# Optimization experiments

Measured on AMD Instinct MI355X. Metric: run time of the kernel, lower is better.

The kernel has to match this reference:

```python
import jax, jax.numpy as jnp
import numpy as np

B, S, H = 8, 2048, 512
DK = 512


def setup_inputs() -> dict:
    key = jax.random.key(0)
    ks = jax.random.split(key, 10)
    inp = {
        "X": jax.random.normal(ks[0], (B, S, H), dtype=jnp.float32),
        "event_flag": jax.random.uniform(ks[1], (B, S, 1), dtype=jnp.float32),
        "lengths": jax.random.randint(ks[2], (B,), 1, S + 1),
        # Linear params (torch Linear: y = x @ W.T + b, W is [out,in])
        "Wq": jax.random.normal(ks[3], (H, H), dtype=jnp.float32) / np.sqrt(H),
        "bq": jnp.zeros((H,), dtype=jnp.float32),
        "Wk": jax.random.normal(ks[4], (H, H), dtype=jnp.float32) / np.sqrt(H),
        "bk": jnp.zeros((H,), dtype=jnp.float32),
        "Wv": jax.random.normal(ks[5], (H, H), dtype=jnp.float32) / np.sqrt(H),
        "bv": jnp.zeros((H,), dtype=jnp.float32),
        "event_weight": jnp.zeros((1,), dtype=jnp.float32),
        "shape_ratio": jnp.ones((1,), dtype=jnp.float32),
    }
    return inp


def reference(X, event_flag, lengths, Wq, bq, Wk, bk, Wv, bv, event_weight, shape_ratio):
    # QKV projections: [B,S,H]
    Q = jnp.einsum("bsh,oh->bso", X, Wq) + bq
    K = jnp.einsum("bsh,oh->bso", X, Wk) + bk
    V = jnp.einsum("bsh,oh->bso", X, Wv) + bv
    # scaled scores [B,S,S], learned shape_ratio scale
    scores = jnp.einsum("bqh,bkh->bqk", Q, K) / jnp.sqrt(jnp.float32(DK))
    scores = scores * shape_ratio
    # event_flag [B,S,1] broadcasts over last (key) dim: per-query additive bias
    scores = scores + event_weight * event_flag
    attn = jax.nn.softmax(scores, axis=-1)
    context = jnp.einsum("bqk,bkh->bqh", attn, V)
    return context, attn
```

## Files before the change

### kernel.cpp

```cpp
#include <hip/hip_runtime.h>
#include <stdint.h>


#define Bn 8
#define Sn 2048
#define Hn 512
#define BM 128
#define BN 128
#define BKk 64

typedef unsigned short u16;
typedef _Float16 h16;
typedef __attribute__((ext_vector_type(8))) _Float16 f16x8;
typedef __attribute__((ext_vector_type(4))) _Float16 f16x4;
typedef __attribute__((ext_vector_type(4))) float f32x4;

__device__ __forceinline__ f32x4 mfma16h(f16x8 a, f16x8 b, f32x4 c) {
  return __builtin_amdgcn_mfma_f32_16x16x32_f16(a, b, c, 0, 0, 0);
}
__device__ __forceinline__ void g2l16(const void* g, void* l) {
  __builtin_amdgcn_global_load_lds(
      (const __attribute__((address_space(1))) void*)g,
      (__attribute__((address_space(3))) void*)l,
      16, 0, 0);
}

__global__ __launch_bounds__(256) void k0_cvt(
    const float* __restrict__ X,
    const float* __restrict__ Wq, const float* __restrict__ Wk,
    const float* __restrict__ Wv,
    h16* __restrict__ Xf, h16* __restrict__ Wf) {
  const int l = blockIdx.x;
  const float* src;
  h16* dst;
  int i;
  if (l < 4096) {
    src = X;
    dst = Xf;
    i = (l * 256 + threadIdx.x) * 8;
  } else {
    const int w = l - 4096;
    const int mat = w >> 7;
    src = (mat == 0) ? Wq : ((mat == 1) ? Wk : Wv);
    dst = Wf + (size_t)mat * 512 * 512;
    i = ((w & 127) * 256 + threadIdx.x) * 8;
  }
  float4 v0 = *(const float4*)(src + i);
  float4 v1 = *(const float4*)(src + i + 4);
  f16x8 h;
  h[0] = (h16)v0.x; h[1] = (h16)v0.y; h[2] = (h16)v0.z; h[3] = (h16)v0.w;
  h[4] = (h16)v1.x; h[5] = (h16)v1.y; h[6] = (h16)v1.z; h[7] = (h16)v1.w;
  *(f16x8*)(dst + i) = h;
}

__global__ __launch_bounds__(256) void k1_proj(
    const h16* __restrict__ Xf, const h16* __restrict__ Wf,
    const float* __restrict__ bq, const float* __restrict__ bk,
    const float* __restrict__ bv,
    h16* __restrict__ Qf, h16* __restrict__ Kf, h16* __restrict__ Vt) {
  __shared__ h16 lA[BM * BKk], lB[BM * BKk];
  const int t = threadIdx.x;
  const int lane = t & 63;
  const int wid = t >> 6;
  const int wr = wid >> 1, wc = wid & 1;
  const int l = blockIdx.x;
  const int xcd = l & 7;
  const int slot = l >> 3;
  const int m_idx = xcd * 16 + slot / 12;
  const int tn = slot % 12;
  const int m0 = m_idx * BM;
  const int mat = tn >> 2;
  const int o0 = (tn & 3) * BN;
  const float* bsel = (mat == 0) ? bq : ((mat == 1) ? bk : bv);
  const size_t arow0 = (size_t)m0;
  const size_t brow0 = (size_t)mat * 512 + o0;

  f32x4 acc[4][4];
  const f32x4 fz = {0.f, 0.f, 0.f, 0.f};
#pragma unroll
  for (int m = 0; m < 4; ++m)
#pragma unroll
    for (int n = 0; n < 4; ++n) acc[m][n] = fz;

  const int srow = lane >> 3;
  const int scol = ((lane & 7) ^ srow) << 3;

  for (int k0 = 0; k0 < Hn; k0 += BKk) {
    __syncthreads();
#pragma unroll
    for (int j = 0; j < 4; ++j) {
      const int ci = wid * 4 + j;
      const int row = ci * 8 + srow;
      g2l16(Xf + (arow0 + row) * Hn + k0 + scol, &lA[ci * 512]);
      g2l16(Wf + (brow0 + row) * Hn + k0 + scol, &lB[ci * 512]);
    }
    __syncthreads();
#pragma unroll
    for (int ks = 0; ks < 2; ++ks) {
      f16x8 af[4], bf[4];
#pragma unroll
      for (int m = 0; m < 4; ++m) {
        const int row = wr * 64 + m * 16 + (lane & 15);
        const int col8 = ks * 4 + (lane >> 4);
        af[m] = *(const f16x8*)&lA[row * BKk + ((col8 ^ (row & 7)) << 3)];
      }
#pragma unroll
      for (int n = 0; n < 4; ++n) {
        const int row = wc * 64 + n * 16 + (lane & 15);
        const int col8 = ks * 4 + (lane >> 4);
        bf[n] = *(const f16x8*)&lB[row * BKk + ((col8 ^ (row & 7)) << 3)];
      }
#pragma unroll
      for (int m = 0; m < 4; ++m)
#pragma unroll
        for (int n = 0; n < 4; ++n)
          acc[m][n] = mfma16h(af[m], bf[n], acc[m][n]);
    }
  }
#pragma unroll
  for (int n = 0; n < 4; ++n) {
    const int o = o0 + wc * 64 + n * 16 + (lane & 15);
    const float bias = bsel[o];
#pragma unroll
    for (int m = 0; m < 4; ++m) {
      const int ib = m0 + wr * 64 + m * 16 + ((lane >> 4) << 2);
      if (mat < 2) {
        h16* Dst = (mat == 0) ? Qf : Kf;
#pragma unroll
        for (int r = 0; r < 4; ++r)
          Dst[(size_t)(ib + r) * Hn + o] = (h16)(acc[m][n][r] + bias);
      } else {
        const int bb = ib >> 11, s = ib & 2047;
        f16x4 p;
#pragma unroll
        for (int r = 0; r < 4; ++r) p[r] = (h16)(acc[m][n][r] + bias);
        *(f16x4*)&Vt[((size_t)bb * Hn + o) * Sn + s] = p;
      }
    }
  }
}

__global__ __launch_bounds__(256) void k2_scores(
    const h16* __restrict__ Qf, const h16* __restrict__ Kf,
    const float* __restrict__ shape_ratio,
    h16* __restrict__ Ep, size_t estride, int eoff,
    float* __restrict__ Par) {
  __shared__ h16 lA[BM * BKk], lB[BM * BKk];
  const int t = threadIdx.x;
  const int lane = t & 63;
  const int wid = t >> 6;
  const int wr = wid >> 1, wc = wid & 1;
  const int l = blockIdx.x;
  const int b = l & 7;
  const int slot = l >> 3;
  const int mi = slot >> 4;
  const int ni = slot & 15;
  const int n0 = ni * BN;
  const int m0 = mi * BM;
  const size_t qrow0 = (size_t)b * Sn + m0;
  const size_t krow0 = (size_t)b * Sn + n0;

  f32x4 acc[4][4];
  const f32x4 fz = {0.f, 0.f, 0.f, 0.f};
#pragma unroll
  for (int m = 0; m < 4; ++m)
#pragma unroll
    for (int n = 0; n < 4; ++n) acc[m][n] = fz;

  const int srow = lane >> 3;
  const int scol = ((lane & 7) ^ srow) << 3;

  for (int k0 = 0; k0 < Hn; k0 += BKk) {
    __syncthreads();
#pragma unroll
    for (int j = 0; j < 4; ++j) {
      const int ci = wid * 4 + j;
      const int row = ci * 8 + srow;
      g2l16(Qf + (qrow0 + row) * Hn + k0 + scol, &lA[ci * 512]);
      g2l16(Kf + (krow0 + row) * Hn + k0 + scol, &lB[ci * 512]);
    }
    __syncthreads();
#pragma unroll
    for (int ks = 0; ks < 2; ++ks) {
      f16x8 af[4], bf[4];
#pragma unroll
      for (int m = 0; m < 4; ++m) {
        const int row = wr * 64 + m * 16 + (lane & 15);
        const int col8 = ks * 4 + (lane >> 4);
        af[m] = *(const f16x8*)&lA[row * BKk + ((col8 ^ (row & 7)) << 3)];
      }
#pragma unroll
      for (int n = 0; n < 4; ++n) {
        const int row = wc * 64 + n * 16 + (lane & 15);
        const int col8 = ks * 4 + (lane >> 4);
        bf[n] = *(const f16x8*)&lB[row * BKk + ((col8 ^ (row & 7)) << 3)];
      }
#pragma unroll
      for (int m = 0; m < 4; ++m)
#pragma unroll
        for (int n = 0; n < 4; ++n)
          acc[m][n] = mfma16h(af[m], bf[n], acc[m][n]);
    }
  }
  const float scale = shape_ratio[0] * 0.044194173824159216f;
  float psum[4][4];
#pragma unroll
  for (int m = 0; m < 4; ++m)
#pragma unroll
    for (int r = 0; r < 4; ++r) psum[m][r] = 0.f;

#pragma unroll
  for (int n = 0; n < 4; ++n) {
    const int kk = n0 + wc * 64 + n * 16 + (lane & 15);
#pragma unroll
    for (int m = 0; m < 4; ++m) {
      const int q = m0 + wr * 64 + m * 16 + ((lane >> 4) << 2);
#pragma unroll
      for (int r = 0; r < 4; ++r) {
        const float e = __expf(acc[m][n][r] * scale);
        Ep[((size_t)b * Sn + q + r) * estride + eoff + kk] = (h16)e;
        psum[m][r] += e;
      }
    }
  }
#pragma unroll
  for (int m = 0; m < 4; ++m)
#pragma unroll
    for (int r = 0; r < 4; ++r) {
      float s = psum[m][r];
      s += __shfl_xor(s, 1);
      s += __shfl_xor(s, 2);
      s += __shfl_xor(s, 4);
      s += __shfl_xor(s, 8);
      psum[m][r] = s;
    }
  if ((lane & 15) == 0) {
    const int pslot = ni * 2 + wc;
#pragma unroll
    for (int m = 0; m < 4; ++m) {
      const int q = m0 + wr * 64 + m * 16 + ((lane >> 4) << 2);
#pragma unroll
      for (int r = 0; r < 4; ++r)
        Par[((size_t)b * Sn + q + r) * 32 + pslot] = psum[m][r];
    }
  }
}

__global__ __launch_bounds__(256) void k4_pv(
    const h16* __restrict__ Ep, size_t estride, int eoff,
    const float* __restrict__ Par, const h16* __restrict__ Vt,
    float* __restrict__ Ctx) {
  __shared__ h16 lA[2][BM * BKk], lB[2][BM * BKk];
  __shared__ float invSh[BM];
  const int t = threadIdx.x;
  const int lane = t & 63;
  const int wid = t >> 6;
  const int wr = wid >> 1, wc = wid & 1;
  const int l = blockIdx.x;
  const int b = l & 7;
  const int slot = l >> 3;
  const int mi = slot >> 2;
  const int ni = slot & 3;
  const int n0 = ni * BN;
  const int m0 = mi * BM;

  if (t < BM) {
    const float* p = Par + ((size_t)b * Sn + m0 + t) * 32;
    float s = 0.f;
#pragma unroll
    for (int i = 0; i < 32; ++i) s += p[i];
    invSh[t] = 1.0f / s;
  }

  f32x4 acc[4][4];
  const f32x4 fz = {0.f, 0.f, 0.f, 0.f};
#pragma unroll
  for (int m = 0; m < 4; ++m)
#pragma unroll
    for (int n = 0; n < 4; ++n) acc[m][n] = fz;

  const int srow = lane >> 3;
  const int scol = ((lane & 7) ^ srow) << 3;

  auto stage = [&](int bufi, int k0) {
#pragma unroll
    for (int j = 0; j < 4; ++j) {
      const int ci = wid * 4 + j;
      const int row = ci * 8 + srow;
      g2l16(Ep + ((size_t)(b * Sn + m0 + row)) * estride + eoff + k0 + scol,
            &lA[bufi][ci * 512]);
      g2l16(Vt + ((size_t)b * Hn + n0 + row) * Sn + k0 + scol,
            &lB[bufi][ci * 512]);
    }
  };

  stage(0, 0);
  __syncthreads();
  int cur = 0;
  for (int tt = 0; tt < Sn / BKk; ++tt) {
    if (tt + 1 < Sn / BKk) stage(cur ^ 1, (tt + 1) * BKk);
#pragma unroll
    for (int ks = 0; ks < 2; ++ks) {
      f16x8 af[4], bf[4];
#pragma unroll
      for (int m = 0; m < 4; ++m) {
        const int row = wr * 64 + m * 16 + (lane & 15);
        const int col8 = ks * 4 + (lane >> 4);
        af[m] = *(const f16x8*)&lA[cur][row * BKk + ((col8 ^ (row & 7)) << 3)];
      }
#pragma unroll
      for (int n = 0; n < 4; ++n) {
        const int row = wc * 64 + n * 16 + (lane & 15);
        const int col8 = ks * 4 + (lane >> 4);
        bf[n] = *(const f16x8*)&lB[cur][row * BKk + ((col8 ^ (row & 7)) << 3)];
      }
#pragma unroll
      for (int m = 0; m < 4; ++m)
#pragma unroll
        for (int n = 0; n < 4; ++n)
          acc[m][n] = mfma16h(af[m], bf[n], acc[m][n]);
    }
    __syncthreads();
    cur ^= 1;
  }
#pragma unroll
  for (int n = 0; n < 4; ++n) {
    const int h = n0 + wc * 64 + n * 16 + (lane & 15);
#pragma unroll
    for (int m = 0; m < 4; ++m) {
      const int qb = wr * 64 + m * 16 + ((lane >> 4) << 2);
#pragma unroll
      for (int r = 0; r < 4; ++r)
        Ctx[((size_t)(b * Sn + m0 + qb + r)) * Hn + h] =
            acc[m][n][r] * invSh[qb + r];
    }
  }
}

__global__ __launch_bounds__(256) void k3_norm(
    const h16* __restrict__ Ep, size_t estride, int eoff,
    const float* __restrict__ Par, float* __restrict__ attnF) {
  const int r = blockIdx.x;
  const int t = threadIdx.x;
  float* row = attnF + (size_t)r * Sn;
  const h16* erow = Ep + (size_t)r * estride + eoff;

  f16x8 e = *(const f16x8*)(erow + t * 8);

  __shared__ float shInv;
  float s = (t < 32) ? Par[(size_t)r * 32 + t] : 0.f;
  if (t < 64) {
    s += __shfl_xor(s, 32);
    s += __shfl_xor(s, 16);
    s += __shfl_xor(s, 8);
    s += __shfl_xor(s, 4);
    s += __shfl_xor(s, 2);
    s += __shfl_xor(s, 1);
    if (t == 0) shInv = 1.0f / s;
  }
  __syncthreads();
  const float iv = shInv;

  float4 o0 = make_float4((float)e[0] * iv, (float)e[1] * iv,
                          (float)e[2] * iv, (float)e[3] * iv);
  float4 o1 = make_float4((float)e[4] * iv, (float)e[5] * iv,
                          (float)e[6] * iv, (float)e[7] * iv);
  *(float4*)(row + t * 8) = o0;
  *(float4*)(row + t * 8 + 4) = o1;
}

extern "C" void kernel_launch(void* const* d_in, const int* in_sizes, int n_in,
                              void* d_out, int out_size, void* d_ws, size_t ws_size,
                              hipStream_t stream) {
  const float* X  = (const float*)d_in[0];
  const float* Wq = (const float*)d_in[3];
  const float* bq = (const float*)d_in[4];
  const float* Wk = (const float*)d_in[5];
  const float* bk = (const float*)d_in[6];
  const float* Wv = (const float*)d_in[7];
  const float* bv = (const float*)d_in[8];
  const float* shape_ratio = (const float*)d_in[10];

  float* ctx  = (float*)d_out;
  float* attn = ctx + (size_t)Bn * Sn * Hn;

  h16* ws = (h16*)d_ws;
  const size_t A = (size_t)Bn * Sn * Hn;
  const size_t W3 = (size_t)3 * 512 * 512;
  h16* Xf = ws;
  h16* Wf = ws + A;
  h16* Qf = ws + A + W3;
  h16* Kf = ws + 2 * A + W3;
  float* Par = (float*)(ws + 3 * A + W3);
  h16* Vt = ws + 4 * A;

  const bool bigWs = ws_size >= (size_t)9 * A * 2;

  k0_cvt<<<dim3(4480), 256, 0, stream>>>(X, Wq, Wk, Wv, Xf, Wf);
  k1_proj<<<dim3(1536), 256, 0, stream>>>(Xf, Wf, bq, bk, bv, Qf, Kf, Vt);

  if (bigWs) {
    h16* Ep = ws + 5 * A;
    k2_scores<<<dim3(2048), 256, 0, stream>>>(Qf, Kf, shape_ratio,
                                              Ep, (size_t)Sn, 0, Par);
    k4_pv<<<dim3(512), 256, 0, stream>>>(Ep, (size_t)Sn, 0, Par, Vt, ctx);
    k3_norm<<<dim3(Bn * Sn), 256, 0, stream>>>(Ep, (size_t)Sn, 0, Par, attn);
  } else {
    k2_scores<<<dim3(2048), 256, 0, stream>>>(Qf, Kf, shape_ratio,
                                              (h16*)attn, (size_t)4096, 2048,
                                              Par);
    k4_pv<<<dim3(512), 256, 0, stream>>>((const h16*)attn, (size_t)4096, 2048,
                                         Par, Vt, ctx);
    k3_norm<<<dim3(Bn * Sn), 256, 0, stream>>>((const h16*)attn, (size_t)4096,
                                               2048, Par, attn);
  }
}
```

Before: 195.1 us.

## Fuse softmax normalization into scores kernel via last-block atomic counter

```diff
diff --git a/kernel.cpp b/kernel.cpp
--- a/kernel.cpp
+++ b/kernel.cpp
@@ -144,8 +144,10 @@
     const h16* __restrict__ Qf, const h16* __restrict__ Kf,
     const float* __restrict__ shape_ratio,
     h16* __restrict__ Ep, size_t estride, int eoff,
-    float* __restrict__ Par) {
+    float* __restrict__ Par, float* __restrict__ attnF, int* Cnt) {
   __shared__ h16 lA[BM * BKk], lB[BM * BKk];
+  __shared__ int tick;
+  __shared__ float inv2[BM];
   const int t = threadIdx.x;
   const int lane = t & 63;
   const int wid = t >> 6;
@@ -243,6 +245,37 @@
       for (int r = 0; r < 4; ++r)
         Par[((size_t)b * Sn + q + r) * 32 + pslot] = psum[m][r];
     }
+  }
+
+  if (Cnt == nullptr) return;
+
+  __threadfence();
+  if (t == 0) tick = atomicAdd(&Cnt[(b << 4) + mi], 1);
+  __syncthreads();
+  if (tick != 15) return;
+  __threadfence();
+
+  if (t < BM) {
+    const float* p = Par + ((size_t)b * Sn + m0 + t) * 32;
+    float s = 0.f;
+#pragma unroll
+    for (int i = 0; i < 32; ++i) s += p[i];
+    inv2[t] = 1.0f / s;
+  }
+  __syncthreads();
+
+#pragma unroll 2
+  for (int rr = 0; rr < BM; ++rr) {
+    const size_t gr = (size_t)b * Sn + m0 + rr;
+    const float iv = inv2[rr];
+    const f16x8 e = *(const f16x8*)(Ep + gr * estride + eoff + t * 8);
+    float* dst = attnF + gr * Sn + t * 8;
+    float4 o0 = make_float4((float)e[0] * iv, (float)e[1] * iv,
+                            (float)e[2] * iv, (float)e[3] * iv);
+    float4 o1 = make_float4((float)e[4] * iv, (float)e[5] * iv,
+                            (float)e[6] * iv, (float)e[7] * iv);
+    *(float4*)dst = o0;
+    *(float4*)(dst + 4) = o1;
   }
 }
 
@@ -392,6 +425,7 @@
   h16* Qf = ws + A + W3;
   h16* Kf = ws + 2 * A + W3;
   float* Par = (float*)(ws + 3 * A + W3);
+  int* Cnt = (int*)(ws + 3 * A + W3 + 1048576);
   h16* Vt = ws + 4 * A;
 
   const bool bigWs = ws_size >= (size_t)9 * A * 2;
@@ -401,14 +435,15 @@
 
   if (bigWs) {
     h16* Ep = ws + 5 * A;
+    hipMemsetAsync(Cnt, 0, 128 * sizeof(int), stream);
     k2_scores<<<dim3(2048), 256, 0, stream>>>(Qf, Kf, shape_ratio,
-                                              Ep, (size_t)Sn, 0, Par);
+                                              Ep, (size_t)Sn, 0, Par,
+                                              attn, Cnt);
     k4_pv<<<dim3(512), 256, 0, stream>>>(Ep, (size_t)Sn, 0, Par, Vt, ctx);
-    k3_norm<<<dim3(Bn * Sn), 256, 0, stream>>>(Ep, (size_t)Sn, 0, Par, attn);
   } else {
     k2_scores<<<dim3(2048), 256, 0, stream>>>(Qf, Kf, shape_ratio,
                                               (h16*)attn, (size_t)4096, 2048,
-                                              Par);
+                                              Par, nullptr, nullptr);
     k4_pv<<<dim3(512), 256, 0, stream>>>((const h16*)attn, (size_t)4096, 2048,
                                          Par, Vt, ctx);
     k3_norm<<<dim3(Bn * Sn), 256, 0, stream>>>((const h16*)attn, (size_t)4096,
```

Result: slower. 629.8 us (+222.9%).
